# Optimization experiments

Hardware: AMD Instinct MI355X
Metric: run time of the kernel (lower is better)

The kernel has to match this reference:

```python
import jax, jax.numpy as jnp
import numpy as np

N_EDGES = 1_000_000
N_NODES = 100_000
IN_DIM = 64
HID = 128
OUT = 128
LN_EPS = 1e-5


def setup_inputs() -> dict:
    key = jax.random.key(0)
    ks = jax.random.split(key, 12)
    s = 1.0 / np.sqrt(3 * IN_DIM)  # matches nn.Linear(3*IN_DIM, HID) init bound
    inp = {
        "efeat": jax.random.normal(ks[0], (N_EDGES, IN_DIM), jnp.float32),
        "src_feat": jax.random.normal(ks[1], (N_NODES, IN_DIM), jnp.float32),
        "dst_feat": jax.random.normal(ks[2], (N_NODES, IN_DIM), jnp.float32),
        "src_idx": jax.random.randint(ks[3], (N_EDGES,), 0, N_NODES, jnp.int32),
        "dst_idx": jax.random.randint(ks[4], (N_EDGES,), 0, N_NODES, jnp.int32),
        # split first-layer weight (as in TMLPDGL: one Linear split into 3 blocks)
        "W_efeat": jax.random.uniform(ks[5], (HID, IN_DIM), jnp.float32, -s, s),
        "W_src": jax.random.uniform(ks[6], (HID, IN_DIM), jnp.float32, -s, s),
        "W_dst": jax.random.uniform(ks[7], (HID, IN_DIM), jnp.float32, -s, s),
        "b1": jax.random.uniform(ks[8], (HID,), jnp.float32, -s, s),
        "W_out": jax.random.uniform(ks[9], (OUT, HID), jnp.float32, -1.0 / np.sqrt(HID), 1.0 / np.sqrt(HID)),
        "b_out": jax.random.uniform(ks[10], (OUT,), jnp.float32, -1.0 / np.sqrt(HID), 1.0 / np.sqrt(HID)),
        "ln_gamma": jnp.ones((OUT,), jnp.float32),
        "ln_beta": jnp.zeros((OUT,), jnp.float32),
    }
    return inp


def _layernorm(x, gamma, beta):
    mu = jnp.mean(x, axis=-1, keepdims=True)
    var = jnp.mean(jnp.square(x - mu), axis=-1, keepdims=True)
    return (x - mu) * jax.lax.rsqrt(var + LN_EPS) * gamma + beta


def reference(efeat, src_feat, dst_feat, src_idx, dst_idx,
              W_efeat, W_src, W_dst, b1, W_out, b_out, ln_gamma, ln_beta):
    # project each input with its weight block (concat+Linear == sum of projections)
    mlp_efeat = efeat @ W_efeat.T                      # [E, HID]
    mlp_src = src_feat @ W_src.T                       # [N, HID]
    mlp_dst = dst_feat @ W_dst.T + b1                  # [N, HID] (bias once, as in F.linear)
    # sum_efeat_dgl: gather node projections to edges and add
    h = mlp_efeat + mlp_src[src_idx] + mlp_dst[dst_idx]  # [E, HID]
    h = jax.nn.silu(h)
    h = h @ W_out.T + b_out                            # [E, OUT]
    return _layernorm(h, ln_gamma, ln_beta)
```

## Files before the change

kernel.cpp:

```cpp
#include <hip/hip_runtime.h>

#define NE 1000000
#define NNODE 100000

typedef __attribute__((ext_vector_type(8))) _Float16 half8;
typedef __attribute__((ext_vector_type(4))) float f32x4;


__global__ void k_convw(const float* __restrict__ Wef, const float* __restrict__ Wsrc,
                        const float* __restrict__ Wdst, const float* __restrict__ Wout,
                        _Float16* __restrict__ wsh) {
    int i = blockIdx.x * 256 + threadIdx.x;
    if (i < 8192)        wsh[i] = (_Float16)Wef[i];
    else if (i < 16384)  wsh[i] = (_Float16)Wsrc[i - 8192];
    else if (i < 24576)  wsh[i] = (_Float16)Wdst[i - 16384];
    else if (i < 40960)  wsh[i] = (_Float16)Wout[i - 24576];
}

__global__ __launch_bounds__(256) void k_nodeproj(
    const float* __restrict__ src_feat, const float* __restrict__ dst_feat,
    const _Float16* __restrict__ Wsrc16, const _Float16* __restrict__ Wdst16,
    const float* __restrict__ b1,
    _Float16* __restrict__ Psrc, _Float16* __restrict__ Pdst)
{
    const int t = threadIdx.x;
    const bool isDst = (blockIdx.y != 0);
    const float* feat = isDst ? dst_feat : src_feat;
    const _Float16* W = isDst ? Wdst16 : Wsrc16;
    _Float16* P = isDst ? Pdst : Psrc;
    const int base = blockIdx.x * 64;

    __shared__ _Float16 sW[128 * 64];
    __shared__ _Float16 sH[64 * 128];

#pragma unroll
    for (int it = 0; it < 4; ++it) {
        int c = it * 256 + t;
        int row = c >> 3, k8 = c & 7;
        *reinterpret_cast<uint4*>(&sW[row * 64 + ((k8 ^ (row & 7)) << 3)]) =
            reinterpret_cast<const uint4*>(W)[c];
    }
    __syncthreads();

    const int lane = t & 63, wid = t >> 6, l15 = lane & 15, g = lane >> 4;
    const int rb = wid * 16;
    int fr = base + rb + l15; if (fr >= NNODE) fr = NNODE - 1;

    f32x4 acc[8];
#pragma unroll
    for (int nt = 0; nt < 8; ++nt) acc[nt] = {0.f, 0.f, 0.f, 0.f};
#pragma unroll
    for (int ks = 0; ks < 2; ++ks) {
        const float* ap = &feat[(size_t)fr * 64 + ks * 32 + g * 8];
        float4 v0 = *reinterpret_cast<const float4*>(ap);
        float4 v1 = *reinterpret_cast<const float4*>(ap + 4);
        half8 a = { (_Float16)v0.x, (_Float16)v0.y, (_Float16)v0.z, (_Float16)v0.w,
                    (_Float16)v1.x, (_Float16)v1.y, (_Float16)v1.z, (_Float16)v1.w };
        int kb = ks * 4 + g;
#pragma unroll
        for (int nt = 0; nt < 8; ++nt) {
            int row = nt * 16 + l15;
            half8 b = *reinterpret_cast<const half8*>(&sW[row * 64 + ((kb ^ (row & 7)) << 3)]);
            acc[nt] = __builtin_amdgcn_mfma_f32_16x16x32_f16(a, b, acc[nt], 0, 0, 0);
        }
    }
#pragma unroll
    for (int nt = 0; nt < 8; ++nt) {
#pragma unroll
        for (int r = 0; r < 4; ++r) {
            int row = rb + g * 4 + r;
            int col = nt * 16 + l15;
            int k8 = col >> 3, e = col & 7;
            sH[row * 128 + ((k8 ^ (row & 7)) << 3) + e] = (_Float16)acc[nt][r];
        }
    }
    __syncthreads();

    {
        int r2 = t >> 2, q2 = t & 3;
        int orow = base + r2;
        if (orow < NNODE) {
#pragma unroll
            for (int i = 0; i < 4; ++i) {
                int k8 = q2 * 4 + i;
                half8 h = *reinterpret_cast<const half8*>(&sH[r2 * 128 + ((k8 ^ (r2 & 7)) << 3)]);
                if (isDst) {
#pragma unroll
                    for (int j = 0; j < 8; ++j)
                        h[j] = (_Float16)((float)h[j] + b1[k8 * 8 + j]);
                }
                *reinterpret_cast<half8*>(&P[(size_t)orow * 128 + k8 * 8]) = h;
            }
        }
    }
}

__global__ __launch_bounds__(256, 2) void k_edge(
    const float* __restrict__ efeat,
    const int* __restrict__ src_idx, const int* __restrict__ dst_idx,
    const _Float16* __restrict__ Wef16, const _Float16* __restrict__ Wout16,
    const _Float16* __restrict__ Psrc, const _Float16* __restrict__ Pdst,
    const float* __restrict__ b_out, const float* __restrict__ gamma_,
    const float* __restrict__ beta_, float* __restrict__ out)
{
    __shared__ __align__(16) char smem[65536];
    _Float16* sW1 = reinterpret_cast<_Float16*>(smem);
    _Float16* sW2 = reinterpret_cast<_Float16*>(smem + 16384);
    _Float16* sH  = reinterpret_cast<_Float16*>(smem + 49152);
    float*    sLN = reinterpret_cast<float*>(smem);

    const int t = threadIdx.x;
    const size_t base = (size_t)blockIdx.x * 64;
    const int lane = t & 63, wid = t >> 6, l15 = lane & 15, g = lane >> 4;
    const int rb = wid * 16;
    const int r2 = t >> 2, q2 = t & 3;

    size_t eidx = base + r2; if (eidx >= NE) eidx = NE - 1;
    int si = src_idx[eidx];
    int di = dst_idx[eidx];
    uint4 ps[4], pd[4];
    {
        const uint4* Ps4 = reinterpret_cast<const uint4*>(Psrc + (size_t)si * 128);
        const uint4* Pd4 = reinterpret_cast<const uint4*>(Pdst + (size_t)di * 128);
#pragma unroll
        for (int i = 0; i < 4; ++i) { ps[i] = Ps4[q2 * 4 + i]; pd[i] = Pd4[q2 * 4 + i]; }
    }

#pragma unroll
    for (int it = 0; it < 4; ++it) {
        int c = it * 256 + t;
        int row = c >> 3, k8 = c & 7;
        *reinterpret_cast<uint4*>(&sW1[row * 64 + ((k8 ^ (row & 7)) << 3)]) =
            reinterpret_cast<const uint4*>(Wef16)[c];
    }
#pragma unroll
    for (int it = 0; it < 8; ++it) {
        int c = it * 256 + t;
        int row = c >> 4, k8 = c & 15;
        *reinterpret_cast<uint4*>(&sW2[row * 128 + ((k8 ^ (row & 7)) << 3)]) =
            reinterpret_cast<const uint4*>(Wout16)[c];
    }
    __syncthreads();

    size_t er = base + rb + l15; if (er >= NE) er = NE - 1;
    f32x4 acc[8];
#pragma unroll
    for (int nt = 0; nt < 8; ++nt) acc[nt] = {0.f, 0.f, 0.f, 0.f};
#pragma unroll
    for (int ks = 0; ks < 2; ++ks) {
        const float* ap = &efeat[er * 64 + ks * 32 + g * 8];
        float4 v0 = *reinterpret_cast<const float4*>(ap);
        float4 v1 = *reinterpret_cast<const float4*>(ap + 4);
        half8 a = { (_Float16)v0.x, (_Float16)v0.y, (_Float16)v0.z, (_Float16)v0.w,
                    (_Float16)v1.x, (_Float16)v1.y, (_Float16)v1.z, (_Float16)v1.w };
        int kb = ks * 4 + g;
#pragma unroll
        for (int nt = 0; nt < 8; ++nt) {
            int row = nt * 16 + l15;
            half8 b = *reinterpret_cast<const half8*>(&sW1[row * 64 + ((kb ^ (row & 7)) << 3)]);
            acc[nt] = __builtin_amdgcn_mfma_f32_16x16x32_f16(a, b, acc[nt], 0, 0, 0);
        }
    }
#pragma unroll
    for (int nt = 0; nt < 8; ++nt) {
#pragma unroll
        for (int r = 0; r < 4; ++r) {
            int row = rb + g * 4 + r;
            int col = nt * 16 + l15;
            int k8 = col >> 3, e = col & 7;
            sH[row * 128 + ((k8 ^ (row & 7)) << 3) + e] = (_Float16)acc[nt][r];
        }
    }
    __syncthreads();

#pragma unroll
    for (int i = 0; i < 4; ++i) {
        int k8 = q2 * 4 + i;
        _Float16* hp = &sH[r2 * 128 + ((k8 ^ (r2 & 7)) << 3)];
        half8 h = *reinterpret_cast<const half8*>(hp);
        half8 a = __builtin_bit_cast(half8, ps[i]);
        half8 b = __builtin_bit_cast(half8, pd[i]);
#pragma unroll
        for (int j = 0; j < 8; ++j) {
            float x = (float)h[j] + (float)a[j] + (float)b[j];
            float sg = __builtin_amdgcn_rcpf(1.0f + __expf(-x));
            h[j] = (_Float16)(x * sg);
        }
        *reinterpret_cast<half8*>(hp) = h;
    }
    __syncthreads();

    f32x4 acc2[8];
#pragma unroll
    for (int nt = 0; nt < 8; ++nt) acc2[nt] = {0.f, 0.f, 0.f, 0.f};
#pragma unroll
    for (int ks = 0; ks < 4; ++ks) {
        int row_a = rb + l15;
        int kb = ks * 4 + g;
        half8 a = *reinterpret_cast<const half8*>(&sH[row_a * 128 + ((kb ^ (row_a & 7)) << 3)]);
#pragma unroll
        for (int nt = 0; nt < 8; ++nt) {
            int row = nt * 16 + l15;
            half8 b = *reinterpret_cast<const half8*>(&sW2[row * 128 + ((kb ^ (row & 7)) << 3)]);
            acc2[nt] = __builtin_amdgcn_mfma_f32_16x16x32_f16(a, b, acc2[nt], 0, 0, 0);
        }
    }
    __syncthreads();

    float ga[8], be[8];
#pragma unroll
    for (int nt = 0; nt < 8; ++nt) {
        int col = nt * 16 + l15;
        float bo = b_out[col];
        ga[nt] = gamma_[col]; be[nt] = beta_[col];
#pragma unroll
        for (int r = 0; r < 4; ++r) acc2[nt][r] += bo;
    }
#pragma unroll
    for (int r = 0; r < 4; ++r) {
        float s = 0.f, sq = 0.f;
#pragma unroll
        for (int nt = 0; nt < 8; ++nt) { float x = acc2[nt][r]; s += x; sq += x * x; }
#pragma unroll
        for (int m = 1; m <= 8; m <<= 1) {
            s  += __shfl_xor(s,  m, 64);
            sq += __shfl_xor(sq, m, 64);
        }
        float mean = s * 0.0078125f;
        float var  = sq * 0.0078125f - mean * mean;
        float rstd = __builtin_amdgcn_rsqf(var + 1e-5f);
        int row = rb + g * 4 + r;
#pragma unroll
        for (int nt = 0; nt < 8; ++nt) {
            sLN[row * 132 + nt * 16 + l15] = (acc2[nt][r] - mean) * rstd * ga[nt] + be[nt];
        }
    }
    __syncthreads();

    {
        size_t erow = base + r2;
        if (erow < NE) {
#pragma unroll
            for (int i = 0; i < 8; ++i) {
                float4 v = *reinterpret_cast<const float4*>(&sLN[r2 * 132 + q2 * 32 + i * 4]);
                *reinterpret_cast<float4*>(&out[erow * 128 + q2 * 32 + i * 4]) = v;
            }
        }
    }
}

extern "C" void kernel_launch(void* const* d_in, const int* in_sizes, int n_in,
                              void* d_out, int out_size, void* d_ws, size_t ws_size,
                              hipStream_t stream) {
    const float* efeat    = (const float*)d_in[0];
    const float* src_feat = (const float*)d_in[1];
    const float* dst_feat = (const float*)d_in[2];
    const int*   src_idx  = (const int*)d_in[3];
    const int*   dst_idx  = (const int*)d_in[4];
    const float* W_efeat  = (const float*)d_in[5];
    const float* W_src    = (const float*)d_in[6];
    const float* W_dst    = (const float*)d_in[7];
    const float* b1       = (const float*)d_in[8];
    const float* W_out    = (const float*)d_in[9];
    const float* b_out    = (const float*)d_in[10];
    const float* ln_g     = (const float*)d_in[11];
    const float* ln_b     = (const float*)d_in[12];
    float* out = (float*)d_out;

    _Float16* wsh   = reinterpret_cast<_Float16*>(d_ws);
    _Float16* wWef  = wsh;
    _Float16* wWsrc = wsh + 8192;
    _Float16* wWdst = wsh + 16384;
    _Float16* wWout = wsh + 24576;
    _Float16* Psrc  = wsh + 40960;
    _Float16* Pdst  = Psrc + (size_t)NNODE * 128;

    k_convw<<<160, 256, 0, stream>>>(W_efeat, W_src, W_dst, W_out, wsh);
    dim3 gB(1563, 2);
    k_nodeproj<<<gB, 256, 0, stream>>>(src_feat, dst_feat, wWsrc, wWdst, b1, Psrc, Pdst);
    k_edge<<<15625, 256, 0, stream>>>(efeat, src_idx, dst_idx, wWef, wWout,
                                      Psrc, Pdst, b_out, ln_g, ln_b, out);
}
```

Measured before the change: 896.1 us.

## Read MFMA weights from global memory, drop LDS staging, raise edge-kernel occupancy

Both kernels stop staging the weight matrices in shared memory and load MFMA B-fragments straight from global memory, relying on L1/L2 caching. This shrinks the edge kernel's LDS to 16KB, so the launch bound can rise from 2 to 5 blocks per CU to hide gather and HBM latency. Block barriers are removed because each wave only touches its own rows of sH. LayerNorm results are now written directly from registers as 64-byte row segments instead of being staged through LDS for float4 stores. The costs are extra cache traffic for the repeated weight reads and less coalesced output stores.

Result: slower. 1.091 ms (+21.8%).

```diff
diff --git a/kernel.cpp b/kernel.cpp
--- a/kernel.cpp
+++ b/kernel.cpp
@@ -30,17 +30,7 @@
     _Float16* P = isDst ? Pdst : Psrc;
     const int base = blockIdx.x * 64;
 
-    __shared__ _Float16 sW[128 * 64];
     __shared__ _Float16 sH[64 * 128];
-
-#pragma unroll
-    for (int it = 0; it < 4; ++it) {
-        int c = it * 256 + t;
-        int row = c >> 3, k8 = c & 7;
-        *reinterpret_cast<uint4*>(&sW[row * 64 + ((k8 ^ (row & 7)) << 3)]) =
-            reinterpret_cast<const uint4*>(W)[c];
-    }
-    __syncthreads();
 
     const int lane = t & 63, wid = t >> 6, l15 = lane & 15, g = lane >> 4;
     const int rb = wid * 16;
@@ -60,7 +50,7 @@
 #pragma unroll
         for (int nt = 0; nt < 8; ++nt) {
             int row = nt * 16 + l15;
-            half8 b = *reinterpret_cast<const half8*>(&sW[row * 64 + ((kb ^ (row & 7)) << 3)]);
+            half8 b = *reinterpret_cast<const half8*>(&W[row * 64 + kb * 8]);
             acc[nt] = __builtin_amdgcn_mfma_f32_16x16x32_f16(a, b, acc[nt], 0, 0, 0);
         }
     }
@@ -95,19 +85,15 @@
     }
 }
 
-__global__ __launch_bounds__(256, 2) void k_edge(
+__global__ __launch_bounds__(256, 5) void k_edge(
     const float* __restrict__ efeat,
     const int* __restrict__ src_idx, const int* __restrict__ dst_idx,
-    const _Float16* __restrict__ Wef16, const _Float16* __restrict__ Wout16,
+    const _Float16* __restrict__ W1g, const _Float16* __restrict__ W2g,
     const _Float16* __restrict__ Psrc, const _Float16* __restrict__ Pdst,
     const float* __restrict__ b_out, const float* __restrict__ gamma_,
     const float* __restrict__ beta_, float* __restrict__ out)
 {
-    __shared__ __align__(16) char smem[65536];
-    _Float16* sW1 = reinterpret_cast<_Float16*>(smem);
-    _Float16* sW2 = reinterpret_cast<_Float16*>(smem + 16384);
-    _Float16* sH  = reinterpret_cast<_Float16*>(smem + 49152);
-    float*    sLN = reinterpret_cast<float*>(smem);
+    __shared__ _Float16 sH[64 * 128];
 
     const int t = threadIdx.x;
     const size_t base = (size_t)blockIdx.x * 64;
@@ -126,22 +112,6 @@
         for (int i = 0; i < 4; ++i) { ps[i] = Ps4[q2 * 4 + i]; pd[i] = Pd4[q2 * 4 + i]; }
     }
 
-#pragma unroll
-    for (int it = 0; it < 4; ++it) {
-        int c = it * 256 + t;
-        int row = c >> 3, k8 = c & 7;
-        *reinterpret_cast<uint4*>(&sW1[row * 64 + ((k8 ^ (row & 7)) << 3)]) =
-            reinterpret_cast<const uint4*>(Wef16)[c];
-    }
-#pragma unroll
-    for (int it = 0; it < 8; ++it) {
-        int c = it * 256 + t;
-        int row = c >> 4, k8 = c & 15;
-        *reinterpret_cast<uint4*>(&sW2[row * 128 + ((k8 ^ (row & 7)) << 3)]) =
-            reinterpret_cast<const uint4*>(Wout16)[c];
-    }
-    __syncthreads();
-
     size_t er = base + rb + l15; if (er >= NE) er = NE - 1;
     f32x4 acc[8];
 #pragma unroll
@@ -157,7 +127,7 @@
 #pragma unroll
         for (int nt = 0; nt < 8; ++nt) {
             int row = nt * 16 + l15;
-            half8 b = *reinterpret_cast<const half8*>(&sW1[row * 64 + ((kb ^ (row & 7)) << 3)]);
+            half8 b = *reinterpret_cast<const half8*>(&W1g[row * 64 + kb * 8]);
             acc[nt] = __builtin_amdgcn_mfma_f32_16x16x32_f16(a, b, acc[nt], 0, 0, 0);
         }
     }
@@ -171,7 +141,6 @@
             sH[row * 128 + ((k8 ^ (row & 7)) << 3) + e] = (_Float16)acc[nt][r];
         }
     }
-    __syncthreads();
 
 #pragma unroll
     for (int i = 0; i < 4; ++i) {
@@ -188,7 +157,6 @@
         }
         *reinterpret_cast<half8*>(hp) = h;
     }
-    __syncthreads();
 
     f32x4 acc2[8];
 #pragma unroll
@@ -201,11 +169,10 @@
 #pragma unroll
         for (int nt = 0; nt < 8; ++nt) {
             int row = nt * 16 + l15;
-            half8 b = *reinterpret_cast<const half8*>(&sW2[row * 128 + ((kb ^ (row & 7)) << 3)]);
+            half8 b = *reinterpret_cast<const half8*>(&W2g[row * 128 + kb * 8]);
             acc2[nt] = __builtin_amdgcn_mfma_f32_16x16x32_f16(a, b, acc2[nt], 0, 0, 0);
         }
     }
-    __syncthreads();
 
     float ga[8], be[8];
 #pragma unroll
@@ -229,21 +196,12 @@
         float mean = s * 0.0078125f;
         float var  = sq * 0.0078125f - mean * mean;
         float rstd = __builtin_amdgcn_rsqf(var + 1e-5f);
-        int row = rb + g * 4 + r;
-#pragma unroll
-        for (int nt = 0; nt < 8; ++nt) {
-            sLN[row * 132 + nt * 16 + l15] = (acc2[nt][r] - mean) * rstd * ga[nt] + be[nt];
-        }
-    }
-    __syncthreads();
-
-    {
-        size_t erow = base + r2;
-        if (erow < NE) {
-#pragma unroll
-            for (int i = 0; i < 8; ++i) {
-                float4 v = *reinterpret_cast<const float4*>(&sLN[r2 * 132 + q2 * 32 + i * 4]);
-                *reinterpret_cast<float4*>(&out[erow * 128 + q2 * 32 + i * 4]) = v;
+        size_t row = base + rb + g * 4 + r;
+        if (row < NE) {
+            float* op = &out[row * 128 + l15];
+#pragma unroll
+            for (int nt = 0; nt < 8; ++nt) {
+                op[nt * 16] = (acc2[nt][r] - mean) * rstd * ga[nt] + be[nt];
             }
         }
     }
```
